# Kernel optimization log

Hardware: AMD Instinct MI355X
Metric: run time of the kernel (lower is better)

The kernel has to match this reference:

```python
import jax, jax.numpy as jnp
import numpy as np

K = 16          # gcn_k
NHEAD = 4
C = 256         # feat_dims
EPS = 1e-5
LAYERS = ('gcn', 'cross_attn', 'gcn', 'cross_attn')


def _inorm(x, axes):
    # torch InstanceNorm (affine=False): normalize per (batch, channel) over spatial axes
    mu = jnp.mean(x, axes, keepdims=True)
    var = jnp.var(x, axes, keepdims=True)
    return (x - mu) * jax.lax.rsqrt(var + EPS)


def _lrelu(x):
    return jnp.where(x >= 0, x, 0.2 * x)


def _conv1d(x, W, b=None):
    # 1x1 Conv1d: x (B,Cin,N), W (Cout,Cin)
    y = jnp.einsum('bcn,oc->bon', x, W)
    return y if b is None else y + b[None, :, None]


def _graph_features(feats, coords, k):
    # feats (B,N,Cf), coords (B,N,3) -> (B,N,k,2Cf)  [EdgeConv features]
    sq = jnp.sum(coords * coords, axis=-1)  # (B,N)
    d = sq[:, :, None] + sq[:, None, :] - 2.0 * jnp.einsum('bnc,bmc->bnm', coords, coords)
    _, inds = jax.lax.top_k(-d, k + 1)       # k+1 smallest distances, sorted
    inds = inds[:, :, 1:]                    # drop self
    neigh = jax.vmap(lambda f, i: f[i])(feats, inds)  # (B,N,k,Cf)
    center = jnp.broadcast_to(feats[:, :, None, :], neigh.shape)
    return jnp.concatenate([center, neigh - center], axis=-1)


def _gcn(coords, feats, W1, W2, W3, k):
    # coords (B,3,N), feats (B,C,N) -> (B,C,N)
    c = jnp.transpose(coords, (0, 2, 1))
    f = jnp.transpose(feats, (0, 2, 1))
    g1 = _graph_features(f, c, k)                                   # (B,N,k,2C)
    h1 = _lrelu(_inorm(jnp.einsum('bnkc,oc->bonk', g1, W1), (2, 3)))
    f1 = jnp.max(h1, axis=-1)                                       # (B,C,N)
    g2 = _graph_features(jnp.transpose(f1, (0, 2, 1)), c, k)        # (B,N,k,2C)
    h2 = _lrelu(_inorm(jnp.einsum('bnkc,oc->bonk', g2, W2), (2, 3)))
    f2 = jnp.max(h2, axis=-1)                                       # (B,2C,N)
    f3 = jnp.concatenate([feats, f1, f2], axis=1)                   # (B,4C,N)
    return _lrelu(_inorm(_conv1d(f3, W3), (2,)))


def _cross_attn(f1, f2, Wq, bq, Wk, bk, Wv, bv, Wo, bo, Wm1, bm1, Wm2, bm2, nhead):
    B, Cc, N = f1.shape
    d = Cc // nhead
    # torch reshape (B, C, N) -> (B, d, nhead, N): channel c = dd*nhead + h
    q = _conv1d(f1, Wq, bq).reshape(B, d, nhead, -1)
    k = _conv1d(f2, Wk, bk).reshape(B, d, nhead, -1)
    v = _conv1d(f2, Wv, bv).reshape(B, d, nhead, -1)
    scores = jnp.einsum('bdhn,bdhm->bhnm', q, k) / (d ** 0.5)
    attn = jax.nn.softmax(scores, axis=-1)
    feats = jnp.einsum('bhnm,bdhm->bdhn', attn, v).reshape(B, Cc, -1)
    feats = _conv1d(feats, Wo, bo)
    h = _conv1d(jnp.concatenate([f1, feats], axis=1), Wm1, bm1)
    h = jax.nn.relu(_inorm(h, (2,)))
    return _conv1d(h, Wm2, bm2)


def _forward(coords1, feats1, coords2, feats2, gcn_W1, gcn_W2, gcn_W3, ca):
    for li, name in enumerate(LAYERS):
        i = li // 2  # index into stacked per-block params
        if name == 'gcn':
            feats1 = _gcn(coords1, feats1, gcn_W1[i], gcn_W2[i], gcn_W3[i], K)
            feats2 = _gcn(coords2, feats2, gcn_W1[i], gcn_W2[i], gcn_W3[i], K)
        else:
            p = tuple(t[i] for t in ca)
            feats1 = _cross_attn(feats1, feats2, *p, NHEAD)
            feats2 = _cross_attn(feats2, feats1, *p, NHEAD)
    return feats1, feats2


def setup_inputs() -> dict:
    key = jax.random.key(0)
    ks = jax.random.split(key, 20)
    B, N, M = 2, 2048, 2048
    s = 0.05
    f32 = jnp.float32
    return {
        'coords1': jax.random.normal(ks[0], (B, 3, N), f32),
        'feats1': jax.random.normal(ks[1], (B, C, N), f32),
        'coords2': jax.random.normal(ks[2], (B, 3, M), f32),
        'feats2': jax.random.normal(ks[3], (B, C, M), f32),
        'gcn_W1': jax.random.normal(ks[4], (2, C, 2 * C), f32) * s,
        'gcn_W2': jax.random.normal(ks[5], (2, 2 * C, 2 * C), f32) * s,
        'gcn_W3': jax.random.normal(ks[6], (2, C, 4 * C), f32) * s,
        'ca_Wq': jax.random.normal(ks[7], (2, C, C), f32) * s,
        'ca_bq': jax.random.normal(ks[8], (2, C), f32) * s,
        'ca_Wk': jax.random.normal(ks[9], (2, C, C), f32) * s,
        'ca_bk': jax.random.normal(ks[10], (2, C), f32) * s,
        'ca_Wv': jax.random.normal(ks[11], (2, C, C), f32) * s,
        'ca_bv': jax.random.normal(ks[12], (2, C), f32) * s,
        'ca_Wo': jax.random.normal(ks[13], (2, C, C), f32) * s,
        'ca_bo': jax.random.normal(ks[14], (2, C), f32) * s,
        'ca_Wm1': jax.random.normal(ks[15], (2, 2 * C, 2 * C), f32) * s,
        'ca_bm1': jax.random.normal(ks[16], (2, 2 * C), f32) * s,
        'ca_Wm2': jax.random.normal(ks[17], (2, C, 2 * C), f32) * s,
        'ca_bm2': jax.random.normal(ks[18], (2, C), f32) * s,
    }


def reference(coords1, feats1, coords2, feats2, gcn_W1, gcn_W2, gcn_W3,
              ca_Wq, ca_bq, ca_Wk, ca_bk, ca_Wv, ca_bv, ca_Wo, ca_bo,
              ca_Wm1, ca_bm1, ca_Wm2, ca_bm2):
    ca = (ca_Wq, ca_bq, ca_Wk, ca_bk, ca_Wv, ca_bv, ca_Wo, ca_bo,
          ca_Wm1, ca_bm1, ca_Wm2, ca_bm2)
    return _forward(coords1, feats1, coords2, feats2, gcn_W1, gcn_W2, gcn_W3, ca)
```

## Files before the change

### kernel.cpp

```cpp
#include <hip/hip_runtime.h>


namespace {

constexpr int BB = 2, NPV = 2048, CCH = 256, KNB = 16;
typedef long long i64;
typedef unsigned short u16;
typedef unsigned int u32;
constexpr i64 NSTR  = (i64)NPV * 256;
constexpr i64 NSTR2 = (i64)NPV * 512;
constexpr i64 NSTR4 = (i64)NPV * 1024;
constexpr i64 MB = 1048576;

typedef __attribute__((ext_vector_type(8))) short short8v;
typedef __attribute__((ext_vector_type(4))) float f32x4;

__device__ __forceinline__ float lrelu(float v) { return v >= 0.f ? v : 0.2f * v; }

__device__ __forceinline__ void splitbf(float x, u16& h, u16& l) {
  unsigned u = __float_as_uint(x);
  h = (u16)(u >> 16);
  float hf = __uint_as_float(u & 0xffff0000u);
  l = (u16)(__float_as_uint(x - hf) >> 16);
}

__device__ __forceinline__ u16 f2bf_rn(float x) {
  u32 u = __float_as_uint(x);
  return (u16)((u + 0x7fffu + ((u >> 16) & 1u)) >> 16);
}
__device__ __forceinline__ float bf2f(u16 h) {
  return __uint_as_float((u32)h << 16);
}

__global__ __launch_bounds__(256) void k_diag(float* out, int n, float v) {
  int i = blockIdx.x * 256 + threadIdx.x;
  if (i < n) out[i] = v;
}

__global__ __launch_bounds__(256) void k_setup(
    const float* __restrict__ fa, const float* __restrict__ fb,
    float* __restrict__ Xa, float* __restrict__ Xb,
    const float* __restrict__ W1b, const float* __restrict__ W2b,
    float* __restrict__ UVS,
    const float* __restrict__ Wob, float* __restrict__ WoT,
    const float* __restrict__ Wm1b_, float* __restrict__ Wfull,
    const float* __restrict__ bm1b_, const float* __restrict__ bob,
    float* __restrict__ bcomb) {
  int blk = blockIdx.x;
  int t = threadIdx.x;
  if (blk < 8192) {
    int gi = blk * 256 + t;
    bool second = gi >= (1 << 20);
    int idx = gi & ((1 << 20) - 1);
    int b = idx >> 19;
    int n = (idx >> 8) & (NPV - 1);
    int c = idx & (CCH - 1);
    const float* f = second ? fb : fa;
    float* X = second ? Xb : Xa;
    X[idx] = f[((i64)b * CCH + c) * NPV + n];
  } else if (blk < 11264) {
    int i = (blk - 8192) * 256 + t;
    int li = i / 393216;
    int r0 = i - li * 393216;
    const float* W1 = W1b + (i64)li * 131072;
    const float* W2 = W2b + (i64)li * 262144;
    float* dst = UVS + (i64)li * 393216;
    if (r0 < 131072) {
      int r = r0 >> 8, c = r0 & 255;
      dst[r0] = (r < 256) ? W1[(i64)r * 512 + c] - W1[(i64)r * 512 + 256 + c]
                          : W1[(i64)(r - 256) * 512 + 256 + c];
    } else {
      int j = r0 - 131072;
      int r = j >> 8, c = j & 255;
      dst[131072 + j] = (r < 512) ? W2[(i64)r * 512 + c] - W2[(i64)r * 512 + 256 + c]
                                  : W2[(i64)(r - 512) * 512 + 256 + c];
    }
  } else if (blk < 11776) {
    int i = (blk - 11264) * 256 + t;
    int li = i >> 16, rem = i & 65535;
    int c = rem >> 8, k = rem & 255;
    WoT[(i64)li * 65536 + c * 256 + k] = Wob[(i64)li * 65536 + k * 256 + c];
  } else if (blk < 12800) {
    int i = (blk - 11776) * 256 + t;
    int li = i >> 17, rem = i & 131071;
    int o = rem >> 8, c = rem & 255;
    Wfull[(i64)li * 262144 + o * 512 + c] = Wm1b_[(i64)li * 262144 + o * 512 + c];
  } else {
    int g = (blk - 12800) * 256 + t;
    int li = g >> 9, o = g & 511;
    const float* wm1 = Wm1b_ + (i64)li * 262144 + (i64)o * 512 + 256;
    const float* bo = bob + (i64)li * 256;
    float acc = bm1b_[(i64)li * 512 + o];
    for (int k = 0; k < 256; k++) acc += wm1[k] * bo[k];
    bcomb[(i64)li * 512 + o] = acc;
  }
}

__global__ __launch_bounds__(1024) void k_knnp(const float* __restrict__ c1,
                                               const float* __restrict__ c2,
                                               int* __restrict__ o1,
                                               int* __restrict__ o2) {
#pragma clang fp contract(off)
  __shared__ float4 csq[NPV];
  __shared__ float md[16 * 17];
  __shared__ int   mi[16 * 17];
  int set = blockIdx.y >> 1, b = blockIdx.y & 1;
  const float* cb = (set ? c2 : c1) + (i64)b * 3 * NPV;
  int* ob = (set ? o2 : o1) + (i64)b * NPV * KNB;
  int tid = threadIdx.x;
  for (int m = tid; m < NPV; m += 1024) {
    float x = cb[m], y = cb[NPV + m], z = cb[2 * NPV + m];
    csq[m] = make_float4(x, y, z, x * x + y * y + z * z);
  }
  __syncthreads();
  int w = tid >> 6, lane = tid & 63;
  int p = w & 3, s = w >> 2;
  int n = blockIdx.x * 4 + p;
  float4 cn = csq[n];
  float xn = cn.x, yn = cn.y, zn = cn.z, sn = cn.w;
  float dc[8];
#pragma unroll
  for (int t = 0; t < 8; t++) {
    float4 c = csq[s * 512 + t * 64 + lane];
    float dot = xn * c.x + yn * c.y + zn * c.z;
    dc[t] = (sn + c.w) - 2.0f * dot;
  }
  float wd = -3.4e38f; int wm = -1;
  for (int r = 0; r < KNB + 1; r++) {
    float bd = 3.4e38f; int bm = 0x7fffffff;
#pragma unroll
    for (int t = 0; t < 8; t++) {
      int m = s * 512 + t * 64 + lane;
      float d = dc[t];
      bool valid = (d > wd) || (d == wd && m > wm);
      if (valid && (d < bd || (d == bd && m < bm))) { bd = d; bm = m; }
    }
    for (int mask = 1; mask < 64; mask <<= 1) {
      float od = __shfl_xor(bd, mask);
      int om = __shfl_xor(bm, mask);
      if (od < bd || (od == bd && om < bm)) { bd = od; bm = om; }
    }
    if (lane == 0) { md[w * 17 + r] = bd; mi[w * 17 + r] = bm; }
    wd = bd; wm = bm;
  }
  __syncthreads();
  if (w < 4) {
    int ptr = 0;
    float hd = (lane < 4) ? md[(lane * 4 + w) * 17] : 3.4e38f;
    int   hm = (lane < 4) ? mi[(lane * 4 + w) * 17] : 0x7fffffff;
    int* o = ob + (i64)(blockIdx.x * 4 + w) * KNB;
    for (int r = 0; r < KNB + 1; r++) {
      float bd = hd; int bm = hm;
      for (int mask = 1; mask < 64; mask <<= 1) {
        float od = __shfl_xor(bd, mask);
        int om = __shfl_xor(bm, mask);
        if (od < bd || (od == bd && om < bm)) { bd = od; bm = om; }
      }
      if (r > 0 && lane == 0) o[r - 1] = bm & (NPV - 1);
      if (lane < 4 && hd == bd && hm == bm) {
        ptr++;
        hd = (ptr < 17) ? md[(lane * 4 + w) * 17 + ptr] : 3.4e38f;
        hm = (ptr < 17) ? mi[(lane * 4 + w) * 17 + ptr] : 0x7fffffff;
      }
    }
  }
}

template <bool ANORM, bool ACAT, bool ESTAT, int OMODE>
__global__ __launch_bounds__(256) void k_gemm(
    const float* __restrict__ A, int lda, i64 sA,
    const float* __restrict__ A2,
    const float* __restrict__ W, int ldw, i64 sW,
    const float* __restrict__ bias,
    float* __restrict__ C, int ldc, i64 sC,
    int K, int mode, int act,
    const float* __restrict__ pin, int nchA, float invA,
    float* __restrict__ pout, int ncolsTot,
    int tmode, float* __restrict__ out2) {
  __shared__ __align__(16) u16 Ah[128][36], Al[128][36], Bh[128][36], Bl[128][36];
  __shared__ float mv[512], rv[512];
  __shared__ float cs[128][2];
  int b = blockIdx.z;
  A += (i64)b * sA;
  if (ACAT) A2 += (i64)b * NSTR;
  int m0 = blockIdx.x * 128, n0 = blockIdx.y * 128;
  int tid = threadIdx.x;
  int w = tid >> 6, l = tid & 63;
  int wr = w >> 1, wc = w & 1;
  int lc = l & 15, lq = l >> 4;
  int srow = tid >> 1, skh = (tid & 1) * 16;

  if (ANORM) {
    for (int c = tid; c < K; c += 256) {
      float s = 0.f, ss = 0.f;
      for (int hh = 0; hh < nchA; hh++) {
        s  += pin[((i64)(b * nchA + hh) * K + c) * 2];
        ss += pin[((i64)(b * nchA + hh) * K + c) * 2 + 1];
      }
      float mu = s * invA;
      mv[c] = mu;
      rv[c] = 1.0f / sqrtf(ss * invA - mu * mu + 1e-5f);
    }
    __syncthreads();
  }

  const float* Ap = A + (i64)(m0 + srow) * lda + skh;
  const float* Wp = W + (i64)b * sW + (i64)(n0 + srow) * ldw + skh;

  auto loadA = [&](int kt, float4* v) {
#pragma unroll
    for (int j = 0; j < 4; j++) {
      if (ACAT) {
        int col0 = kt + skh;
        const float* ap = (col0 < 256)
            ? A  + (i64)(m0 + srow) * 256 + col0
            : A2 + (i64)(m0 + srow) * 256 + (col0 - 256);
        v[j] = *(const float4*)(ap + j * 4);
      } else {
        v[j] = *(const float4*)(Ap + kt + j * 4);
      }
    }
  };
  auto loadW = [&](int kt, float4* v) {
#pragma unroll
    for (int j = 0; j < 4; j++) v[j] = *(const float4*)(Wp + kt + j * 4);
  };

  float4 ar[4], wv4[4];
  loadA(0, ar); loadW(0, wv4);

  f32x4 acc[4][4];
#pragma unroll
  for (int i = 0; i < 4; i++)
#pragma unroll
    for (int j = 0; j < 4; j++)
#pragma unroll
      for (int r = 0; r < 4; r++) acc[i][j][r] = 0.f;

  int koff = lq * 8;
  for (int kt = 0; kt < K; kt += 32) {
    __syncthreads();
#pragma unroll
    for (int j = 0; j < 4; j++) {
      float4 a = ar[j];
      if (ANORM) {
        float4 mu = *(const float4*)&mv[kt + skh + j * 4];
        float4 rs = *(const float4*)&rv[kt + skh + j * 4];
        a.x = (a.x - mu.x) * rs.x; a.y = (a.y - mu.y) * rs.y;
        a.z = (a.z - mu.z) * rs.z; a.w = (a.w - mu.w) * rs.w;
        if (act == 1) { a.x = lrelu(a.x); a.y = lrelu(a.y);
                        a.z = lrelu(a.z); a.w = lrelu(a.w); }
        else { a.x = fmaxf(a.x, 0.f); a.y = fmaxf(a.y, 0.f);
               a.z = fmaxf(a.z, 0.f); a.w = fmaxf(a.w, 0.f); }
      }
      u16 h0, h1, h2, h3, l0, l1, l2, l3;
      splitbf(a.x, h0, l0); splitbf(a.y, h1, l1);
      splitbf(a.z, h2, l2); splitbf(a.w, h3, l3);
      *(ushort4*)&Ah[srow][skh + j * 4] = make_ushort4(h0, h1, h2, h3);
      *(ushort4*)&Al[srow][skh + j * 4] = make_ushort4(l0, l1, l2, l3);
      float4 bb = wv4[j];
      splitbf(bb.x, h0, l0); splitbf(bb.y, h1, l1);
      splitbf(bb.z, h2, l2); splitbf(bb.w, h3, l3);
      *(ushort4*)&Bh[srow][skh + j * 4] = make_ushort4(h0, h1, h2, h3);
      *(ushort4*)&Bl[srow][skh + j * 4] = make_ushort4(l0, l1, l2, l3);
    }
    __syncthreads();
    if (kt + 32 < K) { loadA(kt + 32, ar); loadW(kt + 32, wv4); }
    short8v ah[4], al4[4], bh[4], bl4[4];
#pragma unroll
    for (int i = 0; i < 4; i++) {
      int r = wr * 64 + i * 16 + lc;
      ah[i]  = *(const short8v*)&Ah[r][koff];
      al4[i] = *(const short8v*)&Al[r][koff];
    }
#pragma unroll
    for (int j = 0; j < 4; j++) {
      int r = wc * 64 + j * 16 + lc;
      bh[j]  = *(const short8v*)&Bh[r][koff];
      bl4[j] = *(const short8v*)&Bl[r][koff];
    }
#pragma unroll
    for (int i = 0; i < 4; i++) {
#pragma unroll
      for (int j = 0; j < 4; j++) {
        acc[i][j] = __builtin_amdgcn_mfma_f32_16x16x32_bf16(ah[i], bh[j], acc[i][j], 0, 0, 0);
        acc[i][j] = __builtin_amdgcn_mfma_f32_16x16x32_bf16(al4[i], bh[j], acc[i][j], 0, 0, 0);
        acc[i][j] = __builtin_amdgcn_mfma_f32_16x16x32_bf16(ah[i], bl4[j], acc[i][j], 0, 0, 0);
      }
    }
  }

  float sj[4] = {0.f, 0.f, 0.f, 0.f}, ssj[4] = {0.f, 0.f, 0.f, 0.f};
#pragma unroll
  for (int j = 0; j < 4; j++) {
    int col = n0 + wc * 64 + j * 16 + lc;
    float bv = (mode == 0 && bias) ? bias[col] : 0.f;
#pragma unroll
    for (int i = 0; i < 4; i++) {
      int rbase = m0 + wr * 64 + i * 16 + lq * 4;
#pragma unroll
      for (int r = 0; r < 4; r++) {
        int row = rbase + r;
        float v;
        if (OMODE == 1) {
          v = acc[i][j][r];
          ((u16*)C)[(i64)b * sC + (i64)row * ldc + col] = f2bf_rn(v);
        } else {
          float* cp = &C[(i64)b * sC + (i64)row * ldc + col];
          v = acc[i][j][r] + ((mode == 0) ? bv : *cp);
          if (tmode != 2) *cp = v;
          if (tmode != 0)
            out2[(i64)b * 524288 + (i64)col * 2048 + row] = v;
        }
        if (ESTAT) { sj[j] += v; ssj[j] += v * v; }
      }
    }
  }
  if (ESTAT) {
#pragma unroll
    for (int j = 0; j < 4; j++) {
      sj[j]  += __shfl_xor(sj[j], 16);  sj[j]  += __shfl_xor(sj[j], 32);
      ssj[j] += __shfl_xor(ssj[j], 16); ssj[j] += __shfl_xor(ssj[j], 32);
    }
    __syncthreads();
    if (wr == 0 && lq == 0) {
#pragma unroll
      for (int j = 0; j < 4; j++) {
        int cl = wc * 64 + j * 16 + lc;
        cs[cl][0] = sj[j]; cs[cl][1] = ssj[j];
      }
    }
    __syncthreads();
    if (wr == 1 && lq == 0) {
#pragma unroll
      for (int j = 0; j < 4; j++) {
        int cl = wc * 64 + j * 16 + lc;
        cs[cl][0] += sj[j]; cs[cl][1] += ssj[j];
      }
    }
    __syncthreads();
    if (tid < 128) {
      i64 slot = ((i64)(b * gridDim.x + blockIdx.x) * ncolsTot + n0 + tid) * 2;
      pout[slot] = cs[tid][0];
      pout[slot + 1] = cs[tid][1];
    }
  }
}

__global__ __launch_bounds__(256) void k_qkv(
    const float* __restrict__ XA, const float* __restrict__ XB,
    const float* __restrict__ Wq, const float* __restrict__ Wk,
    const float* __restrict__ Wv,
    const float* __restrict__ bq, const float* __restrict__ bk,
    const float* __restrict__ bv,
    float* __restrict__ Qp, float* __restrict__ Kp, float* __restrict__ Vp) {
  __shared__ __align__(16) u16 Ah[128][36], Al[128][36], Bh[128][36], Bl[128][36];
  int z = blockIdx.z;
  int mat = z >> 1, b = z & 1;
  const float* A = (mat == 0 ? XA : XB) + (i64)b * NSTR;
  const float* W = (mat == 0 ? Wq : (mat == 1 ? Wk : Wv));
  const float* bias = (mat == 0 ? bq : (mat == 1 ? bk : bv));
  float* C = (mat == 0 ? Qp : (mat == 1 ? Kp : Vp)) + (i64)b * NSTR;
  int m0 = blockIdx.x * 128, n0 = blockIdx.y * 128;
  int tid = threadIdx.x;
  int w = tid >> 6, l = tid & 63;
  int wr = w >> 1, wc = w & 1;
  int lc = l & 15, lq = l >> 4;
  int srow = tid >> 1, skh = (tid & 1) * 16;
  const float* Ap = A + (i64)(m0 + srow) * 256 + skh;
  const float* Wp = W + (i64)(n0 + srow) * 256 + skh;
  float4 ar[4], wv4[4];
#pragma unroll
  for (int j = 0; j < 4; j++) { ar[j] = *(const float4*)(Ap + j * 4);
                                wv4[j] = *(const float4*)(Wp + j * 4); }
  f32x4 acc[4][4];
#pragma unroll
  for (int i = 0; i < 4; i++)
#pragma unroll
    for (int j = 0; j < 4; j++)
#pragma unroll
      for (int r = 0; r < 4; r++) acc[i][j][r] = 0.f;
  int koff = lq * 8;
  for (int kt = 0; kt < 256; kt += 32) {
    __syncthreads();
#pragma unroll
    for (int j = 0; j < 4; j++) {
      u16 h0, h1, h2, h3, l0, l1, l2, l3;
      splitbf(ar[j].x, h0, l0); splitbf(ar[j].y, h1, l1);
      splitbf(ar[j].z, h2, l2); splitbf(ar[j].w, h3, l3);
      *(ushort4*)&Ah[srow][skh + j * 4] = make_ushort4(h0, h1, h2, h3);
      *(ushort4*)&Al[srow][skh + j * 4] = make_ushort4(l0, l1, l2, l3);
      splitbf(wv4[j].x, h0, l0); splitbf(wv4[j].y, h1, l1);
      splitbf(wv4[j].z, h2, l2); splitbf(wv4[j].w, h3, l3);
      *(ushort4*)&Bh[srow][skh + j * 4] = make_ushort4(h0, h1, h2, h3);
      *(ushort4*)&Bl[srow][skh + j * 4] = make_ushort4(l0, l1, l2, l3);
    }
    __syncthreads();
    if (kt + 32 < 256) {
#pragma unroll
      for (int j = 0; j < 4; j++) { ar[j] = *(const float4*)(Ap + kt + 32 + j * 4);
                                    wv4[j] = *(const float4*)(Wp + kt + 32 + j * 4); }
    }
    short8v ah[4], al4[4], bh[4], bl4[4];
#pragma unroll
    for (int i = 0; i < 4; i++) {
      int r = wr * 64 + i * 16 + lc;
      ah[i]  = *(const short8v*)&Ah[r][koff];
      al4[i] = *(const short8v*)&Al[r][koff];
    }
#pragma unroll
    for (int j = 0; j < 4; j++) {
      int r = wc * 64 + j * 16 + lc;
      bh[j]  = *(const short8v*)&Bh[r][koff];
      bl4[j] = *(const short8v*)&Bl[r][koff];
    }
#pragma unroll
    for (int i = 0; i < 4; i++)
#pragma unroll
      for (int j = 0; j < 4; j++) {
        acc[i][j] = __builtin_amdgcn_mfma_f32_16x16x32_bf16(ah[i], bh[j], acc[i][j], 0, 0, 0);
        acc[i][j] = __builtin_amdgcn_mfma_f32_16x16x32_bf16(al4[i], bh[j], acc[i][j], 0, 0, 0);
        acc[i][j] = __builtin_amdgcn_mfma_f32_16x16x32_bf16(ah[i], bl4[j], acc[i][j], 0, 0, 0);
      }
  }
#pragma unroll
  for (int j = 0; j < 4; j++) {
    int col = n0 + wc * 64 + j * 16 + lc;
    float bv = bias[col];
#pragma unroll
    for (int i = 0; i < 4; i++) {
      int rbase = m0 + wr * 64 + i * 16 + lq * 4;
#pragma unroll
      for (int r = 0; r < 4; r++) {
        float v = acc[i][j][r] + bv;
        int row = rbase + r;
        if (mat == 0) C[(i64)row * 256 + col] = v;
        else C[((i64)(col & 3) * 2048 + row) * 64 + (col >> 2)] = v;
      }
    }
  }
}

__global__ __launch_bounds__(256) void k_y3(
    const float* __restrict__ Xbase, const float* __restrict__ F1b,
    const float* __restrict__ F2b, const float* __restrict__ W3b,
    float* __restrict__ Cb,
    const float* __restrict__ pA, const float* __restrict__ pB,
    float* __restrict__ pout, int li) {
  __shared__ __align__(16) u16 Ah[128][36], Al[128][36], Bh[128][36], Bl[128][36];
  __shared__ float mv[1024], rv[1024];
  __shared__ float cs[128][2];
  int z = blockIdx.z;
  const float* X = Xbase + (i64)z * NSTR;
  const float* F1 = F1b + (i64)z * NSTR;
  const float* F2 = F2b + (i64)z * NSTR2;
  const float* W3 = W3b + (i64)li * 262144;
  float* C = Cb + (i64)z * NSTR;
  int m0 = blockIdx.x * 128, n0 = blockIdx.y * 128;
  int tid = threadIdx.x;
  int w = tid >> 6, l = tid & 63;
  int wr = w >> 1, wc = w & 1;
  int lc = l & 15, lq = l >> 4;
  int srow = tid >> 1, skh = (tid & 1) * 16;
  for (int c = tid; c < 768; c += 256) {
    int col = 256 + c;
    const float* P; int cols, idx;
    if (col < 512) { P = pA; cols = 256; idx = col - 256; }
    else           { P = pB; cols = 512; idx = col - 512; }
    float s = 0.f, ss = 0.f;
    for (int hh = 0; hh < 64; hh++) {
      s  += P[((i64)(z * 64 + hh) * cols + idx) * 2];
      ss += P[((i64)(z * 64 + hh) * cols + idx) * 2 + 1];
    }
    float mu = s * (1.f / 32768.f);
    mv[col] = mu;
    rv[col] = 1.0f / sqrtf(ss * (1.f / 32768.f) - mu * mu + 1e-5f);
  }
  __syncthreads();
  auto loadA = [&](int kt, float4* v) {
    int col0 = kt + skh;
    const float* ap;
    if (col0 < 256)      ap = X  + (i64)(m0 + srow) * 256 + col0;
    else if (col0 < 512) ap = F1 + (i64)(m0 + srow) * 256 + (col0 - 256);
    else                 ap = F2 + (i64)(m0 + srow) * 512 + (col0 - 512);
#pragma unroll
    for (int j = 0; j < 4; j++) v[j] = *(const float4*)(ap + j * 4);
  };
  const float* Wp = W3 + (i64)(n0 + srow) * 1024 + skh;
  float4 ar[4], wv4[4];
  loadA(0, ar);
#pragma unroll
  for (int j = 0; j < 4; j++) wv4[j] = *(const float4*)(Wp + j * 4);
  f32x4 acc[4][4];
#pragma unroll
  for (int i = 0; i < 4; i++)
#pragma unroll
    for (int j = 0; j < 4; j++)
#pragma unroll
      for (int r = 0; r < 4; r++) acc[i][j][r] = 0.f;
  int koff = lq * 8;
  for (int kt = 0; kt < 1024; kt += 32) {
    __syncthreads();
    int col0 = kt + skh;
#pragma unroll
    for (int j = 0; j < 4; j++) {
      float4 a = ar[j];
      if (col0 >= 256) {
        float4 mu = *(const float4*)&mv[col0 + j * 4];
        float4 rs = *(const float4*)&rv[col0 + j * 4];
        a.x = lrelu((a.x - mu.x) * rs.x);
        a.y = lrelu((a.y - mu.y) * rs.y);
        a.z = lrelu((a.z - mu.z) * rs.z);
        a.w = lrelu((a.w - mu.w) * rs.w);
      }
      u16 h0, h1, h2, h3, l0, l1, l2, l3;
      splitbf(a.x, h0, l0); splitbf(a.y, h1, l1);
      splitbf(a.z, h2, l2); splitbf(a.w, h3, l3);
      *(ushort4*)&Ah[srow][skh + j * 4] = make_ushort4(h0, h1, h2, h3);
      *(ushort4*)&Al[srow][skh + j * 4] = make_ushort4(l0, l1, l2, l3);
      splitbf(wv4[j].x, h0, l0); splitbf(wv4[j].y, h1, l1);
      splitbf(wv4[j].z, h2, l2); splitbf(wv4[j].w, h3, l3);
      *(ushort4*)&Bh[srow][skh + j * 4] = make_ushort4(h0, h1, h2, h3);
      *(ushort4*)&Bl[srow][skh + j * 4] = make_ushort4(l0, l1, l2, l3);
    }
    __syncthreads();
    if (kt + 32 < 1024) {
      loadA(kt + 32, ar);
#pragma unroll
      for (int j = 0; j < 4; j++) wv4[j] = *(const float4*)(Wp + kt + 32 + j * 4);
    }
    short8v ah[4], al4[4], bh[4], bl4[4];
#pragma unroll
    for (int i = 0; i < 4; i++) {
      int r = wr * 64 + i * 16 + lc;
      ah[i]  = *(const short8v*)&Ah[r][koff];
      al4[i] = *(const short8v*)&Al[r][koff];
    }
#pragma unroll
    for (int j = 0; j < 4; j++) {
      int r = wc * 64 + j * 16 + lc;
      bh[j]  = *(const short8v*)&Bh[r][koff];
      bl4[j] = *(const short8v*)&Bl[r][koff];
    }
#pragma unroll
    for (int i = 0; i < 4; i++)
#pragma unroll
      for (int j = 0; j < 4; j++) {
        acc[i][j] = __builtin_amdgcn_mfma_f32_16x16x32_bf16(ah[i], bh[j], acc[i][j], 0, 0, 0);
        acc[i][j] = __builtin_amdgcn_mfma_f32_16x16x32_bf16(al4[i], bh[j], acc[i][j], 0, 0, 0);
        acc[i][j] = __builtin_amdgcn_mfma_f32_16x16x32_bf16(ah[i], bl4[j], acc[i][j], 0, 0, 0);
      }
  }
  float sj[4] = {0.f, 0.f, 0.f, 0.f}, ssj[4] = {0.f, 0.f, 0.f, 0.f};
#pragma unroll
  for (int j = 0; j < 4; j++) {
    int col = n0 + wc * 64 + j * 16 + lc;
#pragma unroll
    for (int i = 0; i < 4; i++) {
      int rbase = m0 + wr * 64 + i * 16 + lq * 4;
#pragma unroll
      for (int r = 0; r < 4; r++) {
        float v = acc[i][j][r];
        C[(i64)(rbase + r) * 256 + col] = v;
        sj[j] += v; ssj[j] += v * v;
      }
    }
  }
#pragma unroll
  for (int j = 0; j < 4; j++) {
    sj[j]  += __shfl_xor(sj[j], 16);  sj[j]  += __shfl_xor(sj[j], 32);
    ssj[j] += __shfl_xor(ssj[j], 16); ssj[j] += __shfl_xor(ssj[j], 32);
  }
  __syncthreads();
  if (wr == 0 && lq == 0) {
#pragma unroll
    for (int j = 0; j < 4; j++) {
      int cl = wc * 64 + j * 16 + lc;
      cs[cl][0] = sj[j]; cs[cl][1] = ssj[j];
    }
  }
  __syncthreads();
  if (wr == 1 && lq == 0) {
#pragma unroll
    for (int j = 0; j < 4; j++) {
      int cl = wc * 64 + j * 16 + lc;
      cs[cl][0] += sj[j]; cs[cl][1] += ssj[j];
    }
  }
  __syncthreads();
  if (tid < 128) {
    i64 slot = ((i64)(z * 16 + blockIdx.x) * 256 + n0 + tid) * 2;
    pout[slot] = cs[tid][0];
    pout[slot + 1] = cs[tid][1];
  }
}

template <bool BF16IN>
__global__ __launch_bounds__(256) void k_gstat(const void* __restrict__ Pv,
                                               const void* __restrict__ Qv,
                                               int ldpq,
                                               const int* __restrict__ knn,
                                               int O, float* __restrict__ RM,
                                               float* __restrict__ part) {
  int b = blockIdx.z;
  int o = blockIdx.x * 256 + threadIdx.x;
  int n0 = blockIdx.y * 32;
  RM += (i64)b * 2048 * O;
  knn += ((i64)b * 2048 + n0) * KNB;
  __shared__ int js[32 * KNB];
  for (int i = threadIdx.x; i < 32 * KNB; i += 256) js[i] = knn[i];
  __syncthreads();
  i64 base = (i64)b * 2048 * ldpq;
  float s = 0.f, ss = 0.f;
  for (int r = 0; r < 32; r++) {
    int n = n0 + r;
    float p = BF16IN ? bf2f(((const u16*)Pv)[base + (i64)n * ldpq + o])
                     : ((const float*)Pv)[base + (i64)n * ldpq + o];
    float qm = -3.4e38f, qs = 0.f, qss = 0.f;
#pragma unroll
    for (int k = 0; k < KNB; k++) {
      i64 qoff = base + (i64)js[r * KNB + k] * ldpq + o;
      float q = BF16IN ? bf2f(((const u16*)Qv)[qoff]) : ((const float*)Qv)[qoff];
      qm = fmaxf(qm, q); qs += q; qss += q * q;
    }
    RM[(i64)n * O + o] = p + qm;
    s  += 16.f * p + qs;
    ss += 16.f * p * p + 2.f * p * qs + qss;
  }
  i64 slot = ((i64)b * 64 + blockIdx.y) * O + o;
  part[slot * 2] = s; part[slot * 2 + 1] = ss;
}

__global__ __launch_bounds__(256) void k_normP(const float* __restrict__ src,
                                               float* __restrict__ dst, int cols,
                                               const float* __restrict__ part,
                                               int nch, float inv, int act) {
  int b = blockIdx.z;
  i64 n = blockIdx.x;
  int c = blockIdx.y * 256 + threadIdx.x;
  float s = 0.f, ss = 0.f;
  for (int h = 0; h < nch; h++) {
    s  += part[((i64)(b * nch + h) * cols + c) * 2];
    ss += part[((i64)(b * nch + h) * cols + c) * 2 + 1];
  }
  float mu = s * inv;
  float rs = 1.0f / sqrtf(ss * inv - mu * mu + 1e-5f);
  i64 off = ((i64)b * 2048 + n) * cols + c;
  float v = (src[off] - mu) * rs;
  dst[off] = (act == 1) ? lrelu(v) : fmaxf(v, 0.f);
}

__global__ __launch_bounds__(256) void k_flash(const float* __restrict__ Qp,
                                               const float* __restrict__ Kp,
                                               const float* __restrict__ Vp,
                                               float* __restrict__ Op) {
  __shared__ __align__(16) u16 Kh[64][76], Kl[64][76];
  __shared__ __align__(16) u16 Vh[64][76], Vl[64][76];
  __shared__ __align__(16) u16 Ph[4][16][76], Pl[4][16][76];
  int qt = blockIdx.x, h = blockIdx.y, b = blockIdx.z;
  const float* Qb = Qp + (i64)b * NSTR;
  const float* Khm = Kp + (i64)b * NSTR + (i64)h * 131072;
  const float* Vhm = Vp + (i64)b * NSTR + (i64)h * 131072;
  int tid = threadIdx.x;
  int w = tid >> 6, l = tid & 63;
  int lc = l & 15, lq = l >> 4;
  short8v qh[2], ql[2];
  int qrow = qt * 64 + w * 16 + lc;
#pragma unroll
  for (int ks = 0; ks < 2; ks++) {
#pragma unroll
    for (int j = 0; j < 8; j++) {
      float v = Qb[(i64)qrow * 256 + 4 * (ks * 32 + lq * 8 + j) + h];
      u16 hh, ll; splitbf(v, hh, ll);
      qh[ks][j] = (short)hh; ql[ks][j] = (short)ll;
    }
  }
  float m_r[4] = {-3.0e38f, -3.0e38f, -3.0e38f, -3.0e38f};
  float l_r[4] = {0.f, 0.f, 0.f, 0.f};
  f32x4 acc[4];
#pragma unroll
  for (int j = 0; j < 4; j++)
#pragma unroll
    for (int r = 0; r < 4; r++) acc[j][r] = 0.f;

  for (int kt = 0; kt < 32; kt++) {
    __syncthreads();
    {
      const float* Kt = Khm + (i64)kt * 4096;
      const float* Vt = Vhm + (i64)kt * 4096;
#pragma unroll
      for (int q = 0; q < 4; q++) {
        int v = q * 256 + tid;
        int m = v >> 4, d4 = (v & 15) * 4;
        u16 h0, h1, h2, h3, l0, l1, l2, l3;
        float4 kf = *(const float4*)(Kt + (i64)v * 4);
        splitbf(kf.x, h0, l0); splitbf(kf.y, h1, l1);
        splitbf(kf.z, h2, l2); splitbf(kf.w, h3, l3);
        *(ushort4*)&Kh[m][d4] = make_ushort4(h0, h1, h2, h3);
        *(ushort4*)&Kl[m][d4] = make_ushort4(l0, l1, l2, l3);
        float4 vf = *(const float4*)(Vt + (i64)v * 4);
        splitbf(vf.x, h0, l0); splitbf(vf.y, h1, l1);
        splitbf(vf.z, h2, l2); splitbf(vf.w, h3, l3);
        Vh[d4 + 0][m] = h0; Vh[d4 + 1][m] = h1;
        Vh[d4 + 2][m] = h2; Vh[d4 + 3][m] = h3;
        Vl[d4 + 0][m] = l0; Vl[d4 + 1][m] = l1;
        Vl[d4 + 2][m] = l2; Vl[d4 + 3][m] = l3;
      }
    }
    __syncthreads();
    f32x4 s[4];
#pragma unroll
    for (int j = 0; j < 4; j++)
#pragma unroll
      for (int r = 0; r < 4; r++) s[j][r] = 0.f;
#pragma unroll
    for (int ks = 0; ks < 2; ks++) {
      int ko = ks * 32 + lq * 8;
#pragma unroll
      for (int j = 0; j < 4; j++) {
        short8v bh = *(const short8v*)&Kh[j * 16 + lc][ko];
        short8v bl = *(const short8v*)&Kl[j * 16 + lc][ko];
        s[j] = __builtin_amdgcn_mfma_f32_16x16x32_bf16(qh[ks], bh, s[j], 0, 0, 0);
        s[j] = __builtin_amdgcn_mfma_f32_16x16x32_bf16(ql[ks], bh, s[j], 0, 0, 0);
        s[j] = __builtin_amdgcn_mfma_f32_16x16x32_bf16(qh[ks], bl, s[j], 0, 0, 0);
      }
    }
#pragma unroll
    for (int j = 0; j < 4; j++)
#pragma unroll
      for (int r = 0; r < 4; r++) s[j][r] *= 0.125f;
    float rmax[4];
#pragma unroll
    for (int r = 0; r < 4; r++)
      rmax[r] = fmaxf(fmaxf(s[0][r], s[1][r]), fmaxf(s[2][r], s[3][r]));
#pragma unroll
    for (int mask = 1; mask < 16; mask <<= 1)
#pragma unroll
      for (int r = 0; r < 4; r++) rmax[r] = fmaxf(rmax[r], __shfl_xor(rmax[r], mask));
    float fs[4], rsum[4];
#pragma unroll
    for (int r = 0; r < 4; r++) {
      float mn = fmaxf(m_r[r], rmax[r]);
      fs[r] = expf(m_r[r] - mn);
      m_r[r] = mn; rsum[r] = 0.f;
    }
#pragma unroll
    for (int j = 0; j < 4; j++)
#pragma unroll
      for (int r = 0; r < 4; r++) {
        float p = expf(s[j][r] - m_r[r]);
        rsum[r] += p;
        u16 hh, ll; splitbf(p, hh, ll);
        Ph[w][lq * 4 + r][j * 16 + lc] = hh;
        Pl[w][lq * 4 + r][j * 16 + lc] = ll;
      }
#pragma unroll
    for (int mask = 1; mask < 16; mask <<= 1)
#pragma unroll
      for (int r = 0; r < 4; r++) rsum[r] += __shfl_xor(rsum[r], mask);
#pragma unroll
    for (int r = 0; r < 4; r++) l_r[r] = l_r[r] * fs[r] + rsum[r];
#pragma unroll
    for (int j = 0; j < 4; j++)
#pragma unroll
      for (int r = 0; r < 4; r++) acc[j][r] *= fs[r];
#pragma unroll
    for (int ks = 0; ks < 2; ks++) {
      int ko = ks * 32 + lq * 8;
      short8v ph = *(const short8v*)&Ph[w][lc][ko];
      short8v pl = *(const short8v*)&Pl[w][lc][ko];
#pragma unroll
      for (int j = 0; j < 4; j++) {
        short8v bh = *(const short8v*)&Vh[j * 16 + lc][ko];
        short8v bl = *(const short8v*)&Vl[j * 16 + lc][ko];
        acc[j] = __builtin_amdgcn_mfma_f32_16x16x32_bf16(ph, bh, acc[j], 0, 0, 0);
        acc[j] = __builtin_amdgcn_mfma_f32_16x16x32_bf16(pl, bh, acc[j], 0, 0, 0);
        acc[j] = __builtin_amdgcn_mfma_f32_16x16x32_bf16(ph, bl, acc[j], 0, 0, 0);
      }
    }
  }
  float* Ob = Op + (i64)b * NSTR;
#pragma unroll
  for (int j = 0; j < 4; j++) {
    int dd = j * 16 + lc;
#pragma unroll
    for (int r = 0; r < 4; r++) {
      int q = qt * 64 + w * 16 + lq * 4 + r;
      Ob[(i64)q * 256 + 4 * dd + h] = acc[j][r] / l_r[r];
    }
  }
}

}

extern "C" void kernel_launch(void* const* d_in, const int* in_sizes, int n_in,
                              void* d_out, int out_size, void* d_ws, size_t ws_size,
                              hipStream_t stream) {
  float* outp = (float*)d_out;
  auto diag = [&](float v) {
    k_diag<<<dim3((out_size + 255) / 256), dim3(256), 0, stream>>>(outp, out_size, v);
  };

  static const int DSZ[19] = {12288, 1048576, 12288, 1048576, 262144, 524288, 524288,
                              131072, 512, 131072, 512, 131072, 512, 131072, 512,
                              524288, 1024, 262144, 512};
  if (n_in != 19) { diag(1000.f + (float)n_in); return; }
  for (int i = 0; i < 19; i++) {
    if (in_sizes[i] != DSZ[i]) { diag(2000.f + (float)i); return; }
  }
  if (out_size != 2097152) { diag(3000.f); return; }
  constexpr size_t NEED = 50331648;
  if (ws_size < NEED) { diag((float)(ws_size >> 20)); return; }

  char* w = (char*)d_ws;
  float* S0 = (float*)(w + 0);
  float* S1 = (float*)(w + 4 * MB);
  int*   KN1 = (int*)(w + 8 * MB);
  int*   KN2 = (int*)(w + 8 * MB + 262144);
  float* PARTA = (float*)(w + 8912896);
  float* PARTB = (float*)(w + 9437184);
  float* PARTCg = (float*)(w + 10485760);
  float* PARTCa = (float*)(w + 10616832);
  float* BCOMB = (float*)(w + 10747904);
  float* UVS   = (float*)(w + 10752000);
  float* WFULL = (float*)(w + 13897728);
  char* AR = w + 15994880;

  float* WOT = (float*)(AR + 24 * MB);
  float* PQ1 = (float*)(AR);
  u16*   PQ2 = (u16*)(AR);
  float* F2  = (float*)(AR + 16 * MB);
  float* Y3  = (float*)(AR);
  float* F1d = (float*)d_out;
  float* Qp = (float*)(AR);
  float* Kp = (float*)(AR + 4 * MB);
  float* Vp = (float*)(AR + 8 * MB);
  float* Oc = (float*)(AR + 12 * MB);
  float* Hh = (float*)(AR + 16 * MB);

  const float* W1b = (const float*)d_in[4];
  const float* W2b = (const float*)d_in[5];
  const float* W3b = (const float*)d_in[6];
  const float* Wqb = (const float*)d_in[7];   const float* bqb = (const float*)d_in[8];
  const float* Wkb = (const float*)d_in[9];   const float* bkb = (const float*)d_in[10];
  const float* Wvb = (const float*)d_in[11];  const float* bvb = (const float*)d_in[12];
  const float* Wob = (const float*)d_in[13];  const float* bob = (const float*)d_in[14];
  const float* Wm1b = (const float*)d_in[15]; const float* bm1b = (const float*)d_in[16];
  const float* Wm2b = (const float*)d_in[17]; const float* bm2b = (const float*)d_in[18];

  k_knnp<<<dim3(NPV / 4, 4), dim3(1024), 0, stream>>>(
      (const float*)d_in[0], (const float*)d_in[2], KN1, KN2);
  k_setup<<<dim3(12804), dim3(256), 0, stream>>>(
      (const float*)d_in[1], (const float*)d_in[3], S0, S1,
      W1b, W2b, UVS, Wob, WOT, Wm1b, WFULL, bm1b, bob, BCOMB);
  k_gemm<false, false, false, 0><<<dim3(4, 2, 2), dim3(256), 0, stream>>>(
      Wm1b + 256, 512, 262144, nullptr, WOT, 256, 65536, nullptr,
      WFULL + 256, 512, 262144, 256, 0, 0, nullptr, 0, 0.f, nullptr, 0,
      0, nullptr);

  auto gcn = [&](int li) {
    const float* UV1 = UVS + (i64)li * 393216;
    const float* UV2 = UVS + (i64)li * 393216 + 131072;
    k_gemm<false, false, false, 0><<<dim3(16, 4, 4), dim3(256), 0, stream>>>(
        S0, 256, NSTR, nullptr, UV1, 256, 0, nullptr, PQ1, 512, NSTR2, 256, 0, 0,
        nullptr, 0, 0.f, nullptr, 0, 0, nullptr);
    k_gstat<false><<<dim3(1, 64, 4), dim3(256), 0, stream>>>(
        PQ1, PQ1 + 256, 512, KN1, 256, F1d, PARTA);
    k_gemm<true, false, false, 1><<<dim3(16, 8, 4), dim3(256), 0, stream>>>(
        F1d, 256, NSTR, nullptr, UV2, 256, 0, nullptr,
        (float*)PQ2, 1024, NSTR4, 256, 0, 1,
        PARTA, 64, 1.f / 32768.f, nullptr, 0, 0, nullptr);
    k_gstat<true><<<dim3(2, 64, 4), dim3(256), 0, stream>>>(
        PQ2, PQ2 + 512, 1024, KN1, 512, F2, PARTB);
    k_y3<<<dim3(16, 2, 4), dim3(256), 0, stream>>>(S0, F1d, F2, W3b, Y3,
                                                   PARTA, PARTB, PARTCg, li);
    k_normP<<<dim3(2048, 1, 4), dim3(256), 0, stream>>>(Y3, S0, 256, PARTCg, 16,
                                                        1.f / 2048.f, 1);
  };

  auto attn = [&](const float* XA, const float* XB, float* XO, int li,
                  int tmode, float* out2) {
    const float* Wq = Wqb + (i64)li * 65536;   const float* bq = bqb + (i64)li * 256;
    const float* Wk = Wkb + (i64)li * 65536;   const float* bk = bkb + (i64)li * 256;
    const float* Wv = Wvb + (i64)li * 65536;   const float* bv = bvb + (i64)li * 256;
    const float* Wm2 = Wm2b + (i64)li * 131072; const float* bm2 = bm2b + (i64)li * 256;
    k_qkv<<<dim3(16, 2, 6), dim3(256), 0, stream>>>(XA, XB, Wq, Wk, Wv,
                                                    bq, bk, bv, Qp, Kp, Vp);
    k_flash<<<dim3(32, 4, BB), dim3(256), 0, stream>>>(Qp, Kp, Vp, Oc);
    k_gemm<false, true, true, 0><<<dim3(16, 4, 2), dim3(256), 0, stream>>>(
        XA, 256, NSTR, Oc, WFULL + (i64)li * 262144, 512, 0,
        BCOMB + (i64)li * 512, Hh, 512, NSTR2, 512, 0, 0,
        nullptr, 0, 0.f, PARTCa, 512, 0, nullptr);
    k_gemm<true, false, false, 0><<<dim3(16, 2, 2), dim3(256), 0, stream>>>(
        Hh, 512, NSTR2, nullptr, Wm2, 512, 0, bm2, XO, 256, NSTR, 512, 0, 2,
        PARTCa, 16, 1.f / 2048.f, nullptr, 0, tmode, out2);
  };

  gcn(0);
  attn(S0, S1, S0, 0, 0, nullptr);
  attn(S1, S0, S1, 0, 0, nullptr);
  gcn(1);
  attn(S0, S1, S0, 1, 1, outp);
  attn(S1, S0, S1, 1, 2, outp + 1048576);
}
```

Baseline: 1.495 ms.

## Sort per-lane kNN candidates with packed u64 keys and fold Wo into setup

The kNN kernel now packs each distance (as an order-preserving uint key) with its index into a u64, sorts each lane's 8 candidates with a sorting network, and pops the head each round. This replaces the per-round rescan of all candidates with validity checks, and the wave reduction now shuffles a single 64-bit value instead of a float/int pair. Separately, the Wm1·Wo weight product is computed directly inside the setup kernel with a naive per-thread dot loop. That removes the transpose stage and one GEMM launch, but the product now runs as a slow scalar loop.

```diff
diff --git a/kernel.cpp b/kernel.cpp
--- a/kernel.cpp
+++ b/kernel.cpp
@@ -7,6 +7,7 @@
 typedef long long i64;
 typedef unsigned short u16;
 typedef unsigned int u32;
+typedef unsigned long long u64;
 constexpr i64 NSTR  = (i64)NPV * 256;
 constexpr i64 NSTR2 = (i64)NPV * 512;
 constexpr i64 NSTR4 = (i64)NPV * 1024;
@@ -32,6 +33,11 @@
   return __uint_as_float((u32)h << 16);
 }
 
+__device__ __forceinline__ u32 fkey(float f) {
+  u32 u = __float_as_uint(f);
+  return (u & 0x80000000u) ? ~u : (u | 0x80000000u);
+}
+
 __global__ __launch_bounds__(256) void k_diag(float* out, int n, float v) {
   int i = blockIdx.x * 256 + threadIdx.x;
   if (i < n) out[i] = v;
@@ -42,7 +48,7 @@
     float* __restrict__ Xa, float* __restrict__ Xb,
     const float* __restrict__ W1b, const float* __restrict__ W2b,
     float* __restrict__ UVS,
-    const float* __restrict__ Wob, float* __restrict__ WoT,
+    const float* __restrict__ Wob,
     const float* __restrict__ Wm1b_, float* __restrict__ Wfull,
     const float* __restrict__ bm1b_, const float* __restrict__ bob,
     float* __restrict__ bcomb) {
@@ -75,18 +81,22 @@
       dst[131072 + j] = (r < 512) ? W2[(i64)r * 512 + c] - W2[(i64)r * 512 + 256 + c]
                                   : W2[(i64)(r - 512) * 512 + 256 + c];
     }
-  } else if (blk < 11776) {
-    int i = (blk - 11264) * 256 + t;
-    int li = i >> 16, rem = i & 65535;
-    int c = rem >> 8, k = rem & 255;
-    WoT[(i64)li * 65536 + c * 256 + k] = Wob[(i64)li * 65536 + k * 256 + c];
-  } else if (blk < 12800) {
-    int i = (blk - 11776) * 256 + t;
+  } else if (blk < 12288) {
+    int g = blk - 11264;
+    int li = g >> 9, o = g & 511;
+    int c = t;
+    const float* wm1 = Wm1b_ + (i64)li * 262144 + (i64)o * 512 + 256;
+    const float* wo = Wob + (i64)li * 65536;
+    float acc = 0.f;
+    for (int k = 0; k < 256; k++) acc += wm1[k] * wo[k * 256 + c];
+    Wfull[(i64)li * 262144 + (i64)o * 512 + 256 + c] = acc;
+  } else if (blk < 13312) {
+    int i = (blk - 12288) * 256 + t;
     int li = i >> 17, rem = i & 131071;
     int o = rem >> 8, c = rem & 255;
     Wfull[(i64)li * 262144 + o * 512 + c] = Wm1b_[(i64)li * 262144 + o * 512 + c];
   } else {
-    int g = (blk - 12800) * 256 + t;
+    int g = (blk - 13312) * 256 + t;
     int li = g >> 9, o = g & 511;
     const float* wm1 = Wm1b_ + (i64)li * 262144 + (i64)o * 512 + 256;
     const float* bo = bob + (i64)li * 256;
@@ -98,15 +108,14 @@
 
 __global__ __launch_bounds__(1024) void k_knnp(const float* __restrict__ c1,
                                                const float* __restrict__ c2,
-                                               int* __restrict__ o1,
-                                               int* __restrict__ o2) {
+                                               int* __restrict__ knn1,
+                                               int* __restrict__ knn2) {
 #pragma clang fp contract(off)
   __shared__ float4 csq[NPV];
-  __shared__ float md[16 * 17];
-  __shared__ int   mi[16 * 17];
+  __shared__ u64 ml[16 * 17];
   int set = blockIdx.y >> 1, b = blockIdx.y & 1;
   const float* cb = (set ? c2 : c1) + (i64)b * 3 * NPV;
-  int* ob = (set ? o2 : o1) + (i64)b * NPV * KNB;
+  int* ob = (set ? knn2 : knn1) + (i64)b * NPV * KNB;
   int tid = threadIdx.x;
   for (int m = tid; m < NPV; m += 1024) {
     float x = cb[m], y = cb[NPV + m], z = cb[2 * NPV + m];
@@ -118,49 +127,52 @@
   int n = blockIdx.x * 4 + p;
   float4 cn = csq[n];
   float xn = cn.x, yn = cn.y, zn = cn.z, sn = cn.w;
-  float dc[8];
+  u64 q[8];
 #pragma unroll
   for (int t = 0; t < 8; t++) {
-    float4 c = csq[s * 512 + t * 64 + lane];
+    int m = s * 512 + t * 64 + lane;
+    float4 c = csq[m];
     float dot = xn * c.x + yn * c.y + zn * c.z;
-    dc[t] = (sn + c.w) - 2.0f * dot;
-  }
-  float wd = -3.4e38f; int wm = -1;
+    float d = (sn + c.w) - 2.0f * dot;
+    q[t] = ((u64)fkey(d) << 32) | (u32)m;
+  }
+#define KCAS(a, bb) { u64 lo = q[a] < q[bb] ? q[a] : q[bb]; \
+                      u64 hi = q[a] < q[bb] ? q[bb] : q[a]; \
+                      q[a] = lo; q[bb] = hi; }
+  KCAS(0,1) KCAS(2,3) KCAS(4,5) KCAS(6,7)
+  KCAS(0,2) KCAS(1,3) KCAS(4,6) KCAS(5,7)
+  KCAS(1,2) KCAS(5,6)
+  KCAS(0,4) KCAS(1,5) KCAS(2,6) KCAS(3,7)
+  KCAS(2,4) KCAS(3,5)
+  KCAS(1,2) KCAS(3,4) KCAS(5,6)
+#undef KCAS
   for (int r = 0; r < KNB + 1; r++) {
-    float bd = 3.4e38f; int bm = 0x7fffffff;
-#pragma unroll
-    for (int t = 0; t < 8; t++) {
-      int m = s * 512 + t * 64 + lane;
-      float d = dc[t];
-      bool valid = (d > wd) || (d == wd && m > wm);
-      if (valid && (d < bd || (d == bd && m < bm))) { bd = d; bm = m; }
-    }
+    u64 bmin = q[0];
     for (int mask = 1; mask < 64; mask <<= 1) {
-      float od = __shfl_xor(bd, mask);
-      int om = __shfl_xor(bm, mask);
-      if (od < bd || (od == bd && om < bm)) { bd = od; bm = om; }
-    }
-    if (lane == 0) { md[w * 17 + r] = bd; mi[w * 17 + r] = bm; }
-    wd = bd; wm = bm;
+      u64 ov = (u64)__shfl_xor((long long)bmin, mask);
+      if (ov < bmin) bmin = ov;
+    }
+    if (lane == 0) ml[w * 17 + r] = bmin;
+    if (q[0] == bmin) {
+      q[0] = q[1]; q[1] = q[2]; q[2] = q[3]; q[3] = q[4];
+      q[4] = q[5]; q[5] = q[6]; q[6] = q[7]; q[7] = ~0ull;
+    }
   }
   __syncthreads();
   if (w < 4) {
     int ptr = 0;
-    float hd = (lane < 4) ? md[(lane * 4 + w) * 17] : 3.4e38f;
-    int   hm = (lane < 4) ? mi[(lane * 4 + w) * 17] : 0x7fffffff;
+    u64 h = (lane < 4) ? ml[(lane * 4 + w) * 17] : ~0ull;
     int* o = ob + (i64)(blockIdx.x * 4 + w) * KNB;
     for (int r = 0; r < KNB + 1; r++) {
-      float bd = hd; int bm = hm;
+      u64 bmin = h;
       for (int mask = 1; mask < 64; mask <<= 1) {
-        float od = __shfl_xor(bd, mask);
-        int om = __shfl_xor(bm, mask);
-        if (od < bd || (od == bd && om < bm)) { bd = od; bm = om; }
-      }
-      if (r > 0 && lane == 0) o[r - 1] = bm & (NPV - 1);
-      if (lane < 4 && hd == bd && hm == bm) {
+        u64 ov = (u64)__shfl_xor((long long)bmin, mask);
+        if (ov < bmin) bmin = ov;
+      }
+      if (r > 0 && lane == 0) o[r - 1] = (int)(bmin & (u64)(NPV - 1));
+      if (lane < 4 && h == bmin) {
         ptr++;
-        hd = (ptr < 17) ? md[(lane * 4 + w) * 17 + ptr] : 3.4e38f;
-        hm = (ptr < 17) ? mi[(lane * 4 + w) * 17 + ptr] : 0x7fffffff;
+        h = (ptr < 17) ? ml[(lane * 4 + w) * 17 + ptr] : ~0ull;
       }
     }
   }
@@ -826,7 +838,6 @@
   float* WFULL = (float*)(w + 13897728);
   char* AR = w + 15994880;
 
-  float* WOT = (float*)(AR + 24 * MB);
   float* PQ1 = (float*)(AR);
   u16*   PQ2 = (u16*)(AR);
   float* F2  = (float*)(AR + 16 * MB);
@@ -850,13 +861,9 @@
 
   k_knnp<<<dim3(NPV / 4, 4), dim3(1024), 0, stream>>>(
       (const float*)d_in[0], (const float*)d_in[2], KN1, KN2);
-  k_setup<<<dim3(12804), dim3(256), 0, stream>>>(
+  k_setup<<<dim3(13316), dim3(256), 0, stream>>>(
       (const float*)d_in[1], (const float*)d_in[3], S0, S1,
-      W1b, W2b, UVS, Wob, WOT, Wm1b, WFULL, bm1b, bob, BCOMB);
-  k_gemm<false, false, false, 0><<<dim3(4, 2, 2), dim3(256), 0, stream>>>(
-      Wm1b + 256, 512, 262144, nullptr, WOT, 256, 65536, nullptr,
-      WFULL + 256, 512, 262144, 256, 0, 0, nullptr, 0, 0.f, nullptr, 0,
-      0, nullptr);
+      W1b, W2b, UVS, Wob, Wm1b, WFULL, bm1b, bob, BCOMB);
 
   auto gcn = [&](int li) {
     const float* UV1 = UVS + (i64)li * 393216;
```

Measured after the change: 1.376 ms. 8.0% less time.
